# Optimization experiments

Measured on AMD Instinct MI355X. Metric: run time of the kernel, lower is better.

The kernel has to match this reference:

```python
import jax, jax.numpy as jnp
import numpy as np

B, T, S, C, H, F = 8, 1024, 256, 1024, 16, 4096
D = C // H  # head_dim = 64
EPS = 1e-5


def layernorm(x, g, b):
    mu = jnp.mean(x, axis=-1, keepdims=True)
    var = jnp.var(x, axis=-1, keepdims=True)
    return (x - mu) * jax.lax.rsqrt(var + EPS) * g + b


def setup_inputs() -> dict:
    key = jax.random.key(0)
    ks = jax.random.split(key, 16)
    s = lambda fan_in: 1.0 / np.sqrt(fan_in)
    return {
        "x": jax.random.normal(ks[0], (B, T, C), jnp.float32),
        "context": jax.random.normal(ks[1], (B, S, C), jnp.float32),
        # LayerNorms
        "ln1_g": jnp.ones((C,)), "ln1_b": jnp.zeros((C,)),
        "ln2_g": jnp.ones((C,)), "ln2_b": jnp.zeros((C,)),
        "ln3_g": jnp.ones((C,)), "ln3_b": jnp.zeros((C,)),
        # causal self-attention (qkv has no bias, proj has bias)
        "W_qkv": jax.random.normal(ks[2], (C, 3 * C), jnp.float32) * s(C),
        "W_sproj": jax.random.normal(ks[3], (C, C), jnp.float32) * s(C),
        "b_sproj": jnp.zeros((C,)),
        # cross-attention
        "W_q": jax.random.normal(ks[4], (C, C), jnp.float32) * s(C),
        "W_kv": jax.random.normal(ks[5], (C, 2 * C), jnp.float32) * s(C),
        "W_cproj": jax.random.normal(ks[6], (C, C), jnp.float32) * s(C),
        "b_cproj": jnp.zeros((C,)),
        # FFN
        "W_ff1": jax.random.normal(ks[7], (C, F), jnp.float32) * s(C),
        "b_ff1": jnp.zeros((F,)),
        "W_ff2": jax.random.normal(ks[8], (F, C), jnp.float32) * s(F),
        "b_ff2": jnp.zeros((C,)),
    }


def _split_heads(t):  # [B, L, C] -> [B, H, L, D]
    return t.reshape(t.shape[0], t.shape[1], H, D).transpose(0, 2, 1, 3)


def _merge_heads(t):  # [B, H, L, D] -> [B, L, C]
    return t.transpose(0, 2, 1, 3).reshape(t.shape[0], t.shape[2], C)


def gpt_block(x, context, ln1_g, ln1_b, ln2_g, ln2_b, ln3_g, ln3_b,
              W_qkv, W_sproj, b_sproj, W_q, W_kv, W_cproj, b_cproj,
              W_ff1, b_ff1, W_ff2, b_ff2):
    scale = 1.0 / np.sqrt(D)

    # --- causal self-attention (pre-norm) ---
    h = layernorm(x, ln1_g, ln1_b)
    qkv = h @ W_qkv                       # [B, T, 3C]
    q, k, v = jnp.split(qkv, 3, axis=-1)
    q, k, v = _split_heads(q), _split_heads(k), _split_heads(v)
    attn = jnp.einsum("bhtd,bhsd->bhts", q, k) * scale   # [B, H, T, T]
    causal = jnp.tril(jnp.ones((T, T), dtype=bool))
    attn = jnp.where(causal, attn, -jnp.inf)
    attn = jax.nn.softmax(attn, axis=-1)
    out = jnp.einsum("bhts,bhsd->bhtd", attn, v)
    x = x + (_merge_heads(out) @ W_sproj + b_sproj)

    # --- cross-attention (pre-norm) ---
    h = layernorm(x, ln2_g, ln2_b)
    q = _split_heads(h @ W_q)             # [B, H, T, D]
    kv = context @ W_kv                   # [B, S, 2C]
    k, v = jnp.split(kv, 2, axis=-1)
    k, v = _split_heads(k), _split_heads(v)
    attn = jax.nn.softmax(jnp.einsum("bhtd,bhsd->bhts", q, k) * scale, axis=-1)
    out = jnp.einsum("bhts,bhsd->bhtd", attn, v)
    x = x + (_merge_heads(out) @ W_cproj + b_cproj)

    # --- FFN (pre-norm, exact GELU) ---
    h = layernorm(x, ln3_g, ln3_b)
    h = jax.nn.gelu(h @ W_ff1 + b_ff1, approximate=False)
    x = x + (h @ W_ff2 + b_ff2)
    return x


def reference(x, context, ln1_g, ln1_b, ln2_g, ln2_b, ln3_g, ln3_b,
              W_qkv, W_sproj, b_sproj, W_q, W_kv, W_cproj, b_cproj,
              W_ff1, b_ff1, W_ff2, b_ff2):
    return gpt_block(x, context, ln1_g, ln1_b, ln2_g, ln2_b, ln3_g, ln3_b,
                     W_qkv, W_sproj, b_sproj, W_q, W_kv, W_cproj, b_cproj,
                     W_ff1, b_ff1, W_ff2, b_ff2)
```

## Files before the change

### kernel.cpp

```cpp
#include <hip/hip_runtime.h>
#include <math.h>

constexpr int B_ = 8, T_ = 1024, S_ = 256, C_ = 1024, H_ = 16, F_ = 4096, D_ = 64;

typedef __attribute__((ext_vector_type(8))) short bf16x8;
typedef __attribute__((ext_vector_type(8))) unsigned short ushort8;
typedef __attribute__((ext_vector_type(4))) unsigned short ushort4v;
typedef __attribute__((ext_vector_type(4))) float f32x4;

__device__ __forceinline__ unsigned short f2bf(float f) {
  union { float f; unsigned u; } c; c.f = f;
  unsigned u = c.u;
  u += 0x7FFFu + ((u >> 16) & 1u);
  return (unsigned short)(u >> 16);
}

__device__ __forceinline__ void gload16(const void* g, void* l) {
  typedef __attribute__((address_space(3))) unsigned int lds_u32;
  typedef __attribute__((address_space(1))) const unsigned int glb_u32;
  __builtin_amdgcn_global_load_lds((glb_u32*)(size_t)g,
                                   (lds_u32*)(unsigned)(size_t)l, 16, 0, 0);
}

__device__ __forceinline__ float gelu_exact(float v) {
  return 0.5f * v * (1.0f + erff(v * 0.70710678118654752440f));
}

__global__ __launch_bounds__(256) void ln_kernel(
    const float* __restrict__ x, const float* __restrict__ g,
    const float* __restrict__ b, unsigned short* __restrict__ out) {
  const int row = blockIdx.x;
  const int t = threadIdx.x;
  const float4 v = reinterpret_cast<const float4*>(x + (size_t)row * C_)[t];
  float sum = v.x + v.y + v.z + v.w;
  float ss  = v.x * v.x + v.y * v.y + v.z * v.z + v.w * v.w;
#pragma unroll
  for (int o = 1; o < 64; o <<= 1) {
    sum += __shfl_xor(sum, o);
    ss  += __shfl_xor(ss, o);
  }
  __shared__ float s1[4], s2[4];
  const int wid = t >> 6;
  if ((t & 63) == 0) { s1[wid] = sum; s2[wid] = ss; }
  __syncthreads();
  sum = s1[0] + s1[1] + s1[2] + s1[3];
  ss  = s2[0] + s2[1] + s2[2] + s2[3];
  const float inv = 1.0f / (float)C_;
  const float mu  = sum * inv;
  const float var = ss * inv - mu * mu;
  const float rstd = rsqrtf(var + 1e-5f);
  const float4 gg = reinterpret_cast<const float4*>(g)[t];
  const float4 bb = reinterpret_cast<const float4*>(b)[t];
  ushort4v o4;
  o4[0] = f2bf((v.x - mu) * rstd * gg.x + bb.x);
  o4[1] = f2bf((v.y - mu) * rstd * gg.y + bb.y);
  o4[2] = f2bf((v.z - mu) * rstd * gg.z + bb.z);
  o4[3] = f2bf((v.w - mu) * rstd * gg.w + bb.w);
  *reinterpret_cast<ushort4v*>(out + (size_t)row * C_ + t * 4) = o4;
}

__global__ __launch_bounds__(256) void wconvT_kernel(
    const float* __restrict__ W, unsigned short* __restrict__ Wt, int K, int N) {
  __shared__ unsigned short Lt[64][72];
  const int tid = threadIdx.x;
  const int n0 = blockIdx.x * 64, k0 = blockIdx.y * 64;
#pragma unroll
  for (int j = 0; j < 4; ++j) {
    const int kk = j * 16 + (tid >> 4);
    const float4 v = *reinterpret_cast<const float4*>(W + (size_t)(k0 + kk) * N + n0 + (tid & 15) * 4);
    const int nn = (tid & 15) * 4;
    Lt[nn + 0][kk] = f2bf(v.x);
    Lt[nn + 1][kk] = f2bf(v.y);
    Lt[nn + 2][kk] = f2bf(v.z);
    Lt[nn + 3][kk] = f2bf(v.w);
  }
  __syncthreads();
  const int rr = tid >> 3, ck = tid & 7;
#pragma unroll
  for (int j = 0; j < 2; ++j) {
    const int n = j * 32 + rr;
    *reinterpret_cast<ushort8*>(Wt + (size_t)(n0 + n) * K + k0 + ck * 8) =
        *reinterpret_cast<const ushort8*>(&Lt[n][ck * 8]);
  }
}

__global__ __launch_bounds__(256) void f2bf_kernel(
    const float* __restrict__ in, unsigned short* __restrict__ o, int n8) {
  const int i = blockIdx.x * 256 + threadIdx.x;
  if (i < n8) {
    const float4 a = *reinterpret_cast<const float4*>(in + (size_t)i * 8);
    const float4 b = *reinterpret_cast<const float4*>(in + (size_t)i * 8 + 4);
    ushort8 r;
    r[0] = f2bf(a.x); r[1] = f2bf(a.y); r[2] = f2bf(a.z); r[3] = f2bf(a.w);
    r[4] = f2bf(b.x); r[5] = f2bf(b.y); r[6] = f2bf(b.z); r[7] = f2bf(b.w);
    *reinterpret_cast<ushort8*>(o + (size_t)i * 8) = r;
  }
}

__global__ __launch_bounds__(256) void vtrans_kernel(
    const unsigned short* __restrict__ src, unsigned short* __restrict__ dst,
    int ldsrc, int Ts) {
  __shared__ unsigned short Lt[64][72];
  const int tid = threadIdx.x;
  const int bh = blockIdx.y, b = bh >> 4, h = bh & 15;
  const int t0 = blockIdx.x * 64;
  const int rr = tid >> 3, ck = tid & 7;
#pragma unroll
  for (int j = 0; j < 2; ++j) {
    const int t = j * 32 + rr;
    const ushort8 v = *reinterpret_cast<const ushort8*>(
        src + (size_t)(b * Ts + t0 + t) * ldsrc + h * 64 + ck * 8);
#pragma unroll
    for (int e = 0; e < 8; ++e) Lt[ck * 8 + e][t] = v[e];
  }
  __syncthreads();
#pragma unroll
  for (int j = 0; j < 2; ++j) {
    const int d = j * 32 + rr;
    *reinterpret_cast<ushort8*>(dst + ((size_t)bh * 64 + d) * Ts + t0 + ck * 8) =
        *reinterpret_cast<const ushort8*>(&Lt[d][ck * 8]);
  }
}

enum { EPI_NONE = 0, EPI_BIAS_RESID = 1, EPI_BIAS_GELU = 2 };

template <int EPI>
__global__ __launch_bounds__(256) void gemm_bf16(
    const unsigned short* __restrict__ A, const unsigned short* __restrict__ Bt,
    const float* __restrict__ bias, const float* __restrict__ resid,
    void* __restrict__ Cout, int M, int N, int K) {
  __shared__ unsigned short As[128 * 32];
  __shared__ unsigned short Bs[128 * 32];
  const int tid = threadIdx.x;
  const int w = tid >> 6, lane = tid & 63;
  const int ql = lane & 15, g = lane >> 4;
  const int bm = blockIdx.y * 128, bn = blockIdx.x * 128;
  const int wr = w >> 1, wc = w & 1;

  f32x4 acc[4][4] = {};

  const int srow16 = lane >> 2;
  const int skb = lane & 3;

  for (int k0 = 0; k0 < K; k0 += 32) {
#pragma unroll
    for (int i = 0; i < 2; ++i) {
      const int row = i * 64 + w * 16 + srow16;
      const int kb = skb ^ ((row >> 1) & 3);
      gload16(A + (size_t)(bm + row) * K + k0 + kb * 8,
              (void*)(As + (i * 64 + w * 16) * 32));
      gload16(Bt + (size_t)(bn + row) * K + k0 + kb * 8,
              (void*)(Bs + (i * 64 + w * 16) * 32));
    }
    __syncthreads();
    bf16x8 af[4], bfr[4];
#pragma unroll
    for (int f = 0; f < 4; ++f) {
      const int ra = wr * 64 + f * 16 + ql;
      af[f] = *reinterpret_cast<const bf16x8*>(As + ra * 32 + (g ^ ((ra >> 1) & 3)) * 8);
      const int rb = wc * 64 + f * 16 + ql;
      bfr[f] = *reinterpret_cast<const bf16x8*>(Bs + rb * 32 + (g ^ ((rb >> 1) & 3)) * 8);
    }
#pragma unroll
    for (int mf = 0; mf < 4; ++mf)
#pragma unroll
      for (int nf = 0; nf < 4; ++nf)
        acc[mf][nf] = __builtin_amdgcn_mfma_f32_16x16x32_bf16(af[mf], bfr[nf], acc[mf][nf], 0, 0, 0);
    __syncthreads();
  }

  float b4[4];
  if (EPI != EPI_NONE) {
#pragma unroll
    for (int nf = 0; nf < 4; ++nf) b4[nf] = bias[bn + wc * 64 + nf * 16 + ql];
  }
#pragma unroll
  for (int mf = 0; mf < 4; ++mf) {
#pragma unroll
    for (int r = 0; r < 4; ++r) {
      const size_t m = (size_t)(bm + wr * 64 + mf * 16 + g * 4 + r);
      const int ncol = bn + wc * 64 + ql;
      if (EPI == EPI_BIAS_RESID) {
        float* op = (float*)Cout + m * N + ncol;
        const float* rp = resid + m * N + ncol;
#pragma unroll
        for (int nf = 0; nf < 4; ++nf)
          op[nf * 16] = acc[mf][nf][r] + b4[nf] + rp[nf * 16];
      } else {
        unsigned short* op = (unsigned short*)Cout + m * N + ncol;
#pragma unroll
        for (int nf = 0; nf < 4; ++nf) {
          float v = acc[mf][nf][r];
          if (EPI == EPI_BIAS_GELU) v = gelu_exact(v + b4[nf]);
          op[nf * 16] = f2bf(v);
        }
      }
    }
  }
}

template <bool CAUSAL>
__global__ __launch_bounds__(256) void attn_mfma(
    const unsigned short* __restrict__ Qb, const unsigned short* __restrict__ Kb,
    const unsigned short* __restrict__ Vt, unsigned short* __restrict__ Ob,
    int Tk, int ldq, int ldk) {
  __shared__ unsigned short Ks[64 * 64];
  __shared__ unsigned short Vs[64 * 64];
  __shared__ unsigned short Pt[64][72];
  const int tid = threadIdx.x;
  const int w = tid >> 6, lane = tid & 63;
  const int ql = lane & 15, g = lane >> 4;
  const int bh = blockIdx.y, b = bh >> 4, h = bh & 15;
  const int qt = blockIdx.x;
  const int qrow = w * 16 + ql;
  const int qg = qt * 64 + qrow;

  bf16x8 qf0, qf1;
  {
    const unsigned short* qr = Qb + (size_t)(b * T_ + qg) * ldq + h * 64;
    qf0 = *reinterpret_cast<const bf16x8*>(qr + g * 8);
    qf1 = *reinterpret_cast<const bf16x8*>(qr + 32 + g * 8);
  }
  float m_run = -INFINITY, l_run = 0.f;
  f32x4 oacc[4] = {};

  const int nt = CAUSAL ? (qt + 1) : (Tk >> 6);
  const int srow = lane >> 3, skb = lane & 7;

  for (int kt = 0; kt < nt; ++kt) {
#pragma unroll
    for (int i = 0; i < 2; ++i) {
      const int rloc = i * 32 + w * 8 + srow;
      const int kb = skb ^ (rloc & 7);
      gload16(Kb + (size_t)(b * Tk + kt * 64 + rloc) * ldk + h * 64 + kb * 8,
              (void*)(Ks + (i * 32 + w * 8) * 64));
      gload16(Vt + ((size_t)bh * 64 + rloc) * Tk + kt * 64 + kb * 8,
              (void*)(Vs + (i * 32 + w * 8) * 64));
    }
    __syncthreads();

    f32x4 sacc[4] = {};
#pragma unroll
    for (int kf = 0; kf < 4; ++kf) {
      const int kr = kf * 16 + ql;
      const int sw = ql & 7;
      const bf16x8 k0v = *reinterpret_cast<const bf16x8*>(Ks + kr * 64 + ((0 + g) ^ sw) * 8);
      const bf16x8 k1v = *reinterpret_cast<const bf16x8*>(Ks + kr * 64 + ((4 + g) ^ sw) * 8);
      sacc[kf] = __builtin_amdgcn_mfma_f32_16x16x32_bf16(k0v, qf0, sacc[kf], 0, 0, 0);
      sacc[kf] = __builtin_amdgcn_mfma_f32_16x16x32_bf16(k1v, qf1, sacc[kf], 0, 0, 0);
    }

    float sc[4][4];
    float tmax = -INFINITY;
#pragma unroll
    for (int kf = 0; kf < 4; ++kf)
#pragma unroll
      for (int r = 0; r < 4; ++r) {
        float v = sacc[kf][r] * 0.125f;
        if (CAUSAL) {
          const int key = kt * 64 + kf * 16 + g * 4 + r;
          if (key > qg) v = -INFINITY;
        }
        sc[kf][r] = v;
        tmax = fmaxf(tmax, v);
      }
    tmax = fmaxf(tmax, __shfl_xor(tmax, 16));
    tmax = fmaxf(tmax, __shfl_xor(tmax, 32));
    const float mnew = fmaxf(m_run, tmax);
    const float scl = __expf(m_run - mnew);
    float psum = 0.f;
    unsigned short pb[4][4];
#pragma unroll
    for (int kf = 0; kf < 4; ++kf)
#pragma unroll
      for (int r = 0; r < 4; ++r) {
        const float p = __expf(sc[kf][r] - mnew);
        psum += p;
        pb[kf][r] = f2bf(p);
      }
    psum += __shfl_xor(psum, 16);
    psum += __shfl_xor(psum, 32);
    l_run = l_run * scl + psum;
    m_run = mnew;
#pragma unroll
    for (int df = 0; df < 4; ++df)
#pragma unroll
      for (int r = 0; r < 4; ++r) oacc[df][r] *= scl;
#pragma unroll
    for (int kf = 0; kf < 4; ++kf) {
      ushort4v p4; p4[0] = pb[kf][0]; p4[1] = pb[kf][1]; p4[2] = pb[kf][2]; p4[3] = pb[kf][3];
      *reinterpret_cast<ushort4v*>(&Pt[qrow][kf * 16 + g * 4]) = p4;
    }
    __syncthreads();

    const bf16x8 p0 = *reinterpret_cast<const bf16x8*>(&Pt[qrow][g * 8]);
    const bf16x8 p1 = *reinterpret_cast<const bf16x8*>(&Pt[qrow][32 + g * 8]);
#pragma unroll
    for (int df = 0; df < 4; ++df) {
      const int vr = df * 16 + ql;
      const int sw = ql & 7;
      const bf16x8 v0 = *reinterpret_cast<const bf16x8*>(Vs + vr * 64 + ((0 + g) ^ sw) * 8);
      const bf16x8 v1 = *reinterpret_cast<const bf16x8*>(Vs + vr * 64 + ((4 + g) ^ sw) * 8);
      oacc[df] = __builtin_amdgcn_mfma_f32_16x16x32_bf16(v0, p0, oacc[df], 0, 0, 0);
      oacc[df] = __builtin_amdgcn_mfma_f32_16x16x32_bf16(v1, p1, oacc[df], 0, 0, 0);
    }
    __syncthreads();
  }

  const float linv = 1.0f / l_run;
  unsigned short* orow = Ob + (size_t)(b * T_ + qg) * C_ + h * 64;
#pragma unroll
  for (int df = 0; df < 4; ++df)
#pragma unroll
    for (int r = 0; r < 4; ++r)
      orow[df * 16 + g * 4 + r] = f2bf(oacc[df][r] * linv);
}

extern "C" void kernel_launch(void* const* d_in, const int* in_sizes, int n_in,
                              void* d_out, int out_size, void* d_ws, size_t ws_size,
                              hipStream_t stream) {
  const float* x    = (const float*)d_in[0];
  const float* ctx  = (const float*)d_in[1];
  const float* ln1g = (const float*)d_in[2];
  const float* ln1b = (const float*)d_in[3];
  const float* ln2g = (const float*)d_in[4];
  const float* ln2b = (const float*)d_in[5];
  const float* ln3g = (const float*)d_in[6];
  const float* ln3b = (const float*)d_in[7];
  const float* Wqkv = (const float*)d_in[8];
  const float* Wsp  = (const float*)d_in[9];
  const float* bsp  = (const float*)d_in[10];
  const float* Wq   = (const float*)d_in[11];
  const float* Wkv  = (const float*)d_in[12];
  const float* Wcp  = (const float*)d_in[13];
  const float* bcp  = (const float*)d_in[14];
  const float* Wf1  = (const float*)d_in[15];
  const float* bf1  = (const float*)d_in[16];
  const float* Wf2  = (const float*)d_in[17];
  const float* bf2  = (const float*)d_in[18];
  float* out = (float*)d_out;

  char* wsb = (char*)d_ws;
  unsigned short* WqkvT = (unsigned short*)(wsb + 0);
  unsigned short* WspT  = (unsigned short*)(wsb + 6291456);
  unsigned short* WqT   = (unsigned short*)(wsb + 8388608);
  unsigned short* WkvT  = (unsigned short*)(wsb + 10485760);
  unsigned short* WcpT  = (unsigned short*)(wsb + 14680064);
  unsigned short* Wf1T  = (unsigned short*)(wsb + 16777216);
  unsigned short* Wf2T  = (unsigned short*)(wsb + 25165824);
  unsigned short* ctxb  = (unsigned short*)(wsb + 33554432);
  unsigned short* lnout = (unsigned short*)(wsb + 37748736);
  unsigned short* attno = (unsigned short*)(wsb + 54525952);
  char* regA = wsb + 71303168;
  unsigned short* qkvb = (unsigned short*)regA;
  unsigned short* VtS  = (unsigned short*)(regA + 50331648);
  unsigned short* qbuf = (unsigned short*)regA;
  unsigned short* kvb  = (unsigned short*)(regA + 16777216);
  unsigned short* VtC  = (unsigned short*)(regA + 25165824);
  unsigned short* ff1o = (unsigned short*)regA;

  const dim3 blk(256);

  wconvT_kernel<<<dim3(48, 16), blk, 0, stream>>>(Wqkv, WqkvT, 1024, 3072);
  wconvT_kernel<<<dim3(16, 16), blk, 0, stream>>>(Wsp, WspT, 1024, 1024);
  wconvT_kernel<<<dim3(16, 16), blk, 0, stream>>>(Wq, WqT, 1024, 1024);
  wconvT_kernel<<<dim3(32, 16), blk, 0, stream>>>(Wkv, WkvT, 1024, 2048);
  wconvT_kernel<<<dim3(16, 16), blk, 0, stream>>>(Wcp, WcpT, 1024, 1024);
  wconvT_kernel<<<dim3(64, 16), blk, 0, stream>>>(Wf1, Wf1T, 1024, 4096);
  wconvT_kernel<<<dim3(16, 64), blk, 0, stream>>>(Wf2, Wf2T, 4096, 1024);
  f2bf_kernel<<<1024, blk, 0, stream>>>(ctx, ctxb, 262144);

  ln_kernel<<<8192, blk, 0, stream>>>(x, ln1g, ln1b, lnout);
  gemm_bf16<EPI_NONE><<<dim3(24, 64), blk, 0, stream>>>(
      lnout, WqkvT, nullptr, nullptr, qkvb, 8192, 3072, 1024);
  vtrans_kernel<<<dim3(16, 128), blk, 0, stream>>>(qkvb + 2048, VtS, 3072, 1024);
  attn_mfma<true><<<dim3(16, 128), blk, 0, stream>>>(
      qkvb, qkvb + 1024, VtS, attno, 1024, 3072, 3072);
  gemm_bf16<EPI_BIAS_RESID><<<dim3(8, 64), blk, 0, stream>>>(
      attno, WspT, bsp, x, out, 8192, 1024, 1024);

  ln_kernel<<<8192, blk, 0, stream>>>(out, ln2g, ln2b, lnout);
  gemm_bf16<EPI_NONE><<<dim3(8, 64), blk, 0, stream>>>(
      lnout, WqT, nullptr, nullptr, qbuf, 8192, 1024, 1024);
  gemm_bf16<EPI_NONE><<<dim3(16, 16), blk, 0, stream>>>(
      ctxb, WkvT, nullptr, nullptr, kvb, 2048, 2048, 1024);
  vtrans_kernel<<<dim3(4, 128), blk, 0, stream>>>(kvb + 1024, VtC, 2048, 256);
  attn_mfma<false><<<dim3(16, 128), blk, 0, stream>>>(
      qbuf, kvb, VtC, attno, 256, 1024, 2048);
  gemm_bf16<EPI_BIAS_RESID><<<dim3(8, 64), blk, 0, stream>>>(
      attno, WcpT, bcp, out, out, 8192, 1024, 1024);

  ln_kernel<<<8192, blk, 0, stream>>>(out, ln3g, ln3b, lnout);
  gemm_bf16<EPI_BIAS_GELU><<<dim3(32, 64), blk, 0, stream>>>(
      lnout, Wf1T, bf1, nullptr, ff1o, 8192, 4096, 1024);
  gemm_bf16<EPI_BIAS_RESID><<<dim3(8, 64), blk, 0, stream>>>(
      ff1o, Wf2T, bf2, out, out, 8192, 1024, 4096);
}
```

Measured before the change: 740.0 us.

## Double-buffer LDS tiles in GEMM and attention; use tanh-form GELU

The GEMM and attention kernels now have two LDS buffers for the A/B and K/V tiles. The next tile's global-to-LDS load is issued before the current tile's MFMA work, so memory latency can overlap compute. In attention, the mid-iteration barrier becomes an LDS-only wait plus a raw s_barrier, so the in-flight prefetch is not forced to drain. The exact erf GELU is swapped for a sigmoid/tanh approximation, which cuts epilogue cost but departs slightly from the exact-GELU spec. Doubling LDS use may also reduce occupancy.

New measurement: 693.5 us. 6.3% less time.

```diff
diff --git a/kernel.cpp b/kernel.cpp
--- a/kernel.cpp
+++ b/kernel.cpp
@@ -22,8 +22,8 @@
                                    (lds_u32*)(unsigned)(size_t)l, 16, 0, 0);
 }
 
-__device__ __forceinline__ float gelu_exact(float v) {
-  return 0.5f * v * (1.0f + erff(v * 0.70710678118654752440f));
+__device__ __forceinline__ float gelu_fast(float v) {
+  return v / (1.0f + __expf(-1.5957691216057308f * v * (1.0f + 0.044715f * v * v)));
 }
 
 __global__ __launch_bounds__(256) void ln_kernel(
@@ -129,8 +129,8 @@
     const unsigned short* __restrict__ A, const unsigned short* __restrict__ Bt,
     const float* __restrict__ bias, const float* __restrict__ resid,
     void* __restrict__ Cout, int M, int N, int K) {
-  __shared__ unsigned short As[128 * 32];
-  __shared__ unsigned short Bs[128 * 32];
+  __shared__ unsigned short As[2][128 * 32];
+  __shared__ unsigned short Bs[2][128 * 32];
   const int tid = threadIdx.x;
   const int w = tid >> 6, lane = tid & 63;
   const int ql = lane & 15, g = lane >> 4;
@@ -142,32 +142,44 @@
   const int srow16 = lane >> 2;
   const int skb = lane & 3;
 
-  for (int k0 = 0; k0 < K; k0 += 32) {
+  auto STAGE = [&](int bu, int k0) {
 #pragma unroll
     for (int i = 0; i < 2; ++i) {
       const int row = i * 64 + w * 16 + srow16;
       const int kb = skb ^ ((row >> 1) & 3);
       gload16(A + (size_t)(bm + row) * K + k0 + kb * 8,
-              (void*)(As + (i * 64 + w * 16) * 32));
+              (void*)(As[bu] + (i * 64 + w * 16) * 32));
       gload16(Bt + (size_t)(bn + row) * K + k0 + kb * 8,
-              (void*)(Bs + (i * 64 + w * 16) * 32));
-    }
-    __syncthreads();
+              (void*)(Bs[bu] + (i * 64 + w * 16) * 32));
+    }
+  };
+  auto COMPUTE = [&](int bu) {
     bf16x8 af[4], bfr[4];
 #pragma unroll
     for (int f = 0; f < 4; ++f) {
       const int ra = wr * 64 + f * 16 + ql;
-      af[f] = *reinterpret_cast<const bf16x8*>(As + ra * 32 + (g ^ ((ra >> 1) & 3)) * 8);
+      af[f] = *reinterpret_cast<const bf16x8*>(As[bu] + ra * 32 + (g ^ ((ra >> 1) & 3)) * 8);
       const int rb = wc * 64 + f * 16 + ql;
-      bfr[f] = *reinterpret_cast<const bf16x8*>(Bs + rb * 32 + (g ^ ((rb >> 1) & 3)) * 8);
+      bfr[f] = *reinterpret_cast<const bf16x8*>(Bs[bu] + rb * 32 + (g ^ ((rb >> 1) & 3)) * 8);
     }
 #pragma unroll
     for (int mf = 0; mf < 4; ++mf)
 #pragma unroll
       for (int nf = 0; nf < 4; ++nf)
         acc[mf][nf] = __builtin_amdgcn_mfma_f32_16x16x32_bf16(af[mf], bfr[nf], acc[mf][nf], 0, 0, 0);
+  };
+
+  STAGE(0, 0);
+  __syncthreads();
+  int cur = 0;
+  const int NT = K >> 5;
+  for (int t = 0; t < NT - 1; ++t) {
+    STAGE(cur ^ 1, (t + 1) * 32);
+    COMPUTE(cur);
     __syncthreads();
-  }
+    cur ^= 1;
+  }
+  COMPUTE(cur);
 
   float b4[4];
   if (EPI != EPI_NONE) {
@@ -191,7 +203,7 @@
 #pragma unroll
         for (int nf = 0; nf < 4; ++nf) {
           float v = acc[mf][nf][r];
-          if (EPI == EPI_BIAS_GELU) v = gelu_exact(v + b4[nf]);
+          if (EPI == EPI_BIAS_GELU) v = gelu_fast(v + b4[nf]);
           op[nf * 16] = f2bf(v);
         }
       }
@@ -204,8 +216,8 @@
     const unsigned short* __restrict__ Qb, const unsigned short* __restrict__ Kb,
     const unsigned short* __restrict__ Vt, unsigned short* __restrict__ Ob,
     int Tk, int ldq, int ldk) {
-  __shared__ unsigned short Ks[64 * 64];
-  __shared__ unsigned short Vs[64 * 64];
+  __shared__ unsigned short Ks[2][64 * 64];
+  __shared__ unsigned short Vs[2][64 * 64];
   __shared__ unsigned short Pt[64][72];
   const int tid = threadIdx.x;
   const int w = tid >> 6, lane = tid & 63;
@@ -227,25 +239,32 @@
   const int nt = CAUSAL ? (qt + 1) : (Tk >> 6);
   const int srow = lane >> 3, skb = lane & 7;
 
-  for (int kt = 0; kt < nt; ++kt) {
+  auto STAGE_KV = [&](int bu, int kt) {
 #pragma unroll
     for (int i = 0; i < 2; ++i) {
       const int rloc = i * 32 + w * 8 + srow;
       const int kb = skb ^ (rloc & 7);
       gload16(Kb + (size_t)(b * Tk + kt * 64 + rloc) * ldk + h * 64 + kb * 8,
-              (void*)(Ks + (i * 32 + w * 8) * 64));
+              (void*)(Ks[bu] + (i * 32 + w * 8) * 64));
       gload16(Vt + ((size_t)bh * 64 + rloc) * Tk + kt * 64 + kb * 8,
-              (void*)(Vs + (i * 32 + w * 8) * 64));
-    }
-    __syncthreads();
+              (void*)(Vs[bu] + (i * 32 + w * 8) * 64));
+    }
+  };
+
+  STAGE_KV(0, 0);
+  __syncthreads();
+  int cur = 0;
+
+  for (int kt = 0; kt < nt; ++kt) {
+    if (kt + 1 < nt) STAGE_KV(cur ^ 1, kt + 1);
 
     f32x4 sacc[4] = {};
 #pragma unroll
     for (int kf = 0; kf < 4; ++kf) {
       const int kr = kf * 16 + ql;
       const int sw = ql & 7;
-      const bf16x8 k0v = *reinterpret_cast<const bf16x8*>(Ks + kr * 64 + ((0 + g) ^ sw) * 8);
-      const bf16x8 k1v = *reinterpret_cast<const bf16x8*>(Ks + kr * 64 + ((4 + g) ^ sw) * 8);
+      const bf16x8 k0v = *reinterpret_cast<const bf16x8*>(Ks[cur] + kr * 64 + ((0 + g) ^ sw) * 8);
+      const bf16x8 k1v = *reinterpret_cast<const bf16x8*>(Ks[cur] + kr * 64 + ((4 + g) ^ sw) * 8);
       sacc[kf] = __builtin_amdgcn_mfma_f32_16x16x32_bf16(k0v, qf0, sacc[kf], 0, 0, 0);
       sacc[kf] = __builtin_amdgcn_mfma_f32_16x16x32_bf16(k1v, qf1, sacc[kf], 0, 0, 0);
     }
@@ -291,7 +310,8 @@
       ushort4v p4; p4[0] = pb[kf][0]; p4[1] = pb[kf][1]; p4[2] = pb[kf][2]; p4[3] = pb[kf][3];
       *reinterpret_cast<ushort4v*>(&Pt[qrow][kf * 16 + g * 4]) = p4;
     }
-    __syncthreads();
+    asm volatile("s_waitcnt lgkmcnt(0)" ::: "memory");
+    __builtin_amdgcn_s_barrier();
 
     const bf16x8 p0 = *reinterpret_cast<const bf16x8*>(&Pt[qrow][g * 8]);
     const bf16x8 p1 = *reinterpret_cast<const bf16x8*>(&Pt[qrow][32 + g * 8]);
@@ -299,12 +319,13 @@
     for (int df = 0; df < 4; ++df) {
       const int vr = df * 16 + ql;
       const int sw = ql & 7;
-      const bf16x8 v0 = *reinterpret_cast<const bf16x8*>(Vs + vr * 64 + ((0 + g) ^ sw) * 8);
-      const bf16x8 v1 = *reinterpret_cast<const bf16x8*>(Vs + vr * 64 + ((4 + g) ^ sw) * 8);
+      const bf16x8 v0 = *reinterpret_cast<const bf16x8*>(Vs[cur] + vr * 64 + ((0 + g) ^ sw) * 8);
+      const bf16x8 v1 = *reinterpret_cast<const bf16x8*>(Vs[cur] + vr * 64 + ((4 + g) ^ sw) * 8);
       oacc[df] = __builtin_amdgcn_mfma_f32_16x16x32_bf16(v0, p0, oacc[df], 0, 0, 0);
       oacc[df] = __builtin_amdgcn_mfma_f32_16x16x32_bf16(v1, p1, oacc[df], 0, 0, 0);
     }
     __syncthreads();
+    cur ^= 1;
   }
 
   const float linv = 1.0f / l_run;
```
